# Kernel optimization log

Measured on AMD Instinct MI355X. Metric: run time of the kernel, lower is better.

## Reference

```python
import jax, jax.numpy as jnp
import numpy as np

LATENT_DIMENSION = 128
HIDDEN = 1024            # HIDDEN_SIZE + LATENT_DIMENSION
SONG_PIECE_SIZE = 128
SONG_LENGTH = 32768
T_STEPS = SONG_LENGTH // SONG_PIECE_SIZE  # 256
BATCH = 128


def setup_inputs() -> dict:
    key = jax.random.key(0)
    ks = jax.random.split(key, 7)
    s_ih = 1.0 / np.sqrt(HIDDEN)
    return {
        "current_batch_size": BATCH,
        "z": jax.random.normal(ks[0], (BATCH, 1, LATENT_DIMENSION), dtype=jnp.float32),
        "w_ih": jax.random.normal(ks[1], (4 * HIDDEN, LATENT_DIMENSION), dtype=jnp.float32) * s_ih,
        "w_hh": jax.random.normal(ks[2], (4 * HIDDEN, HIDDEN), dtype=jnp.float32) * s_ih,
        "b_ih": jax.random.normal(ks[3], (4 * HIDDEN,), dtype=jnp.float32) * s_ih,
        "b_hh": jax.random.normal(ks[4], (4 * HIDDEN,), dtype=jnp.float32) * s_ih,
        "W_fc": jax.random.normal(ks[5], (SONG_PIECE_SIZE, HIDDEN), dtype=jnp.float32) * s_ih,
        "b_fc": jax.random.normal(ks[6], (SONG_PIECE_SIZE,), dtype=jnp.float32) * s_ih,
    }


def _run(z, w_ih, w_hh, b_ih, b_hh, W_fc, b_fc):
    B = z.shape[0]
    # inputs per step: step 0 is z[:,0,:], remaining steps are zeros
    xs = jnp.concatenate(
        [z[:, 0:1, :].transpose(1, 0, 2),
         jnp.zeros((T_STEPS - 1, B, LATENT_DIMENSION), dtype=z.dtype)], axis=0)  # [T,B,L]
    h0 = jnp.zeros((B, HIDDEN), dtype=z.dtype)
    c0 = jnp.zeros((B, HIDDEN), dtype=z.dtype)

    def cell(carry, x):
        h, c = carry
        gates = x @ w_ih.T + b_ih + h @ w_hh.T + b_hh  # [B, 4H]
        i, f, g, o = jnp.split(gates, 4, axis=-1)       # PyTorch gate order i,f,g,o
        c_new = jax.nn.sigmoid(f) * c + jax.nn.sigmoid(i) * jnp.tanh(g)
        h_new = jax.nn.sigmoid(o) * jnp.tanh(c_new)
        y = h_new @ W_fc.T + b_fc                       # [B, SONG_PIECE_SIZE]
        return (h_new, c_new), y

    _, ys = jax.lax.scan(cell, (h0, c0), xs)            # ys: [T, B, P]
    return ys.transpose(1, 0, 2).reshape(B, SONG_LENGTH)


def reference(current_batch_size, z, w_ih, w_hh, b_ih, b_hh, W_fc, b_fc):
    return _run(z, w_ih, w_hh, b_ih, b_hh, W_fc, b_fc)
```

## Files before the change

kernel.cpp:

```cpp
#include <hip/hip_runtime.h>
#include <stdint.h>

#define BB   128
#define LL   128
#define HH   1024
#define G4   4096
#define TT   256
#define PP   128

#define NSL  64
#define NB   256
#define CARSL 56
#define FLS  32


typedef _Float16 half8  __attribute__((ext_vector_type(8)));
typedef float   floatx4 __attribute__((ext_vector_type(4)));

__device__ __forceinline__ float sigf(float x) {
  x = fminf(fmaxf(x, -30.f), 30.f);
  return 1.f / (1.f + __expf(-x));
}
__device__ __forceinline__ float tanhf_fast(float x) {
  x = fminf(fmaxf(x, -15.f), 15.f);
  float e = __expf(2.f * x);
  return (e - 1.f) / (e + 1.f);
}
__device__ __forceinline__ unsigned short f2h(float x) {
  _Float16 h = (_Float16)x;
  return __builtin_bit_cast(unsigned short, h);
}
__device__ __forceinline__ void store_h(unsigned short* p, float x) {
  __hip_atomic_store(p, f2h(x), __ATOMIC_RELAXED, __HIP_MEMORY_SCOPE_AGENT);
}

template <bool CACHED, int IMM>
__device__ __forceinline__ void ld16(half8& dst, const unsigned short* base) {
  if constexpr (CACHED)
    asm volatile("global_load_dwordx4 %0, %1, off offset:%2 sc0"
                 : "=&v"(dst) : "v"(base), "n"(IMM) : "memory");
  else
    asm volatile("global_load_dwordx4 %0, %1, off offset:%2 sc0 sc1"
                 : "=&v"(dst) : "v"(base), "n"(IMM) : "memory");
}

#define KSTEP(kc, WN)                                                      \
  {                                                                        \
    asm volatile("s_waitcnt vmcnt(%2)"                                     \
                 : "+v"(ap0[(kc) & 15]), "+v"(ap1[(kc) & 15]) : "n"(WN));  \
    half8 a0 = ap0[(kc) & 15], a1 = ap1[(kc) & 15];                        \
    const int sw = ((kc) * 4 + quad) ^ rsw;                                \
    _Pragma("unroll")                                                      \
    for (int nt = 0; nt < NT; ++nt) {                                      \
      half8 b = (nt < NGATE) ? w8[(nt * 16 + l15) * 128 + sw] : fcb[kc];   \
      acc[0][nt] = __builtin_amdgcn_mfma_f32_16x16x32_f16(a0, b, acc[0][nt], 0, 0, 0); \
      acc[1][nt] = __builtin_amdgcn_mfma_f32_16x16x32_f16(a1, b, acc[1][nt], 0, 0, 0); \
    }                                                                      \
    if ((kc) < 16) {                                                       \
      ld16<CACHED, ((kc) + 16) * 64>(ap0[(kc) & 15], p0);                  \
      ld16<CACHED, ((kc) + 16) * 64>(ap1[(kc) & 15], p1);                  \
    }                                                                      \
  }

__device__ __forceinline__ void publish(unsigned* qf, int sl, unsigned v, int lane) {
  asm volatile("s_waitcnt vmcnt(0)" ::: "memory");
  if (lane == 0)
    __hip_atomic_store(qf + sl * FLS, v, __ATOMIC_RELAXED, __HIP_MEMORY_SCOPE_AGENT);
}
__device__ __forceinline__ void waitq(const unsigned* qf, unsigned tgt, int lane) {
  const unsigned* p = qf + lane * FLS;
  int rounds = 0;
  for (;;) {
    unsigned v = __hip_atomic_load(p, __ATOMIC_RELAXED, __HIP_MEMORY_SCOPE_AGENT);
    if (__all(v >= tgt)) break;
    if (rounds < 2) __builtin_amdgcn_s_sleep(1);
    else            __builtin_amdgcn_s_sleep(8);
    ++rounds;
  }
}

__global__ void prep_gates0(const float* __restrict__ z, const float* __restrict__ w_ih,
                            const float* __restrict__ b_ih, const float* __restrict__ b_hh,
                            float* __restrict__ g0) {
  int j = blockIdx.x;
  int b = threadIdx.x;
  const float* zr = z + b * LL;
  const float* wr = w_ih + (size_t)j * LL;
  float s = 0.f;
#pragma unroll 4
  for (int k = 0; k < LL; ++k) s += zr[k] * wr[k];
  g0[(size_t)b * G4 + j] = s + b_ih[j] + b_hh[j];
}

__global__ void prep_weights(const float* __restrict__ w_hh,
                             unsigned short* __restrict__ wbuf) {
  int R = blockIdx.x;
  int sl = R >> 6, rr = R & 63, tile = rr >> 4, nl = rr & 15;
  int g = (tile == 0) ? 0 : (tile == 1) ? 2 : (tile == 2) ? 1 : 3;
  const float* src = w_hh + (size_t)(g * HH + sl * 16 + nl) * HH;
  int rsw = nl & 7;
  unsigned short* dst = wbuf + (size_t)R * HH;
  for (int k = threadIdx.x; k < HH; k += blockDim.x) {
    int dk = (((k >> 3) ^ rsw) << 3) | (k & 7);
    _Float16 v = (_Float16)src[k];
    dst[dk] = __builtin_bit_cast(unsigned short, v);
  }
}

template <bool CACHED, int NT, int NGATE>
__device__ __forceinline__ void gemmK(const unsigned short* __restrict__ hb,
                                      const half8* __restrict__ w8,
                                      const half8 (&fcb)[32],
                                      int au0, int au1,
                                      int quad, int rsw, int l15,
                                      floatx4 acc[2][NT]) {
  const unsigned short* p0 = hb + au0;
  const unsigned short* p1 = hb + au1;
  half8 ap0[16], ap1[16];
  ld16<CACHED, 0>(ap0[0], p0);     ld16<CACHED, 0>(ap1[0], p1);
  ld16<CACHED, 64>(ap0[1], p0);    ld16<CACHED, 64>(ap1[1], p1);
  ld16<CACHED, 128>(ap0[2], p0);   ld16<CACHED, 128>(ap1[2], p1);
  ld16<CACHED, 192>(ap0[3], p0);   ld16<CACHED, 192>(ap1[3], p1);
  ld16<CACHED, 256>(ap0[4], p0);   ld16<CACHED, 256>(ap1[4], p1);
  ld16<CACHED, 320>(ap0[5], p0);   ld16<CACHED, 320>(ap1[5], p1);
  ld16<CACHED, 384>(ap0[6], p0);   ld16<CACHED, 384>(ap1[6], p1);
  ld16<CACHED, 448>(ap0[7], p0);   ld16<CACHED, 448>(ap1[7], p1);
  ld16<CACHED, 512>(ap0[8], p0);   ld16<CACHED, 512>(ap1[8], p1);
  ld16<CACHED, 576>(ap0[9], p0);   ld16<CACHED, 576>(ap1[9], p1);
  ld16<CACHED, 640>(ap0[10], p0);  ld16<CACHED, 640>(ap1[10], p1);
  ld16<CACHED, 704>(ap0[11], p0);  ld16<CACHED, 704>(ap1[11], p1);
  ld16<CACHED, 768>(ap0[12], p0);  ld16<CACHED, 768>(ap1[12], p1);
  ld16<CACHED, 832>(ap0[13], p0);  ld16<CACHED, 832>(ap1[13], p1);
  ld16<CACHED, 896>(ap0[14], p0);  ld16<CACHED, 896>(ap1[14], p1);
  ld16<CACHED, 960>(ap0[15], p0);  ld16<CACHED, 960>(ap1[15], p1);
  KSTEP(0, 30)  KSTEP(1, 30)  KSTEP(2, 30)  KSTEP(3, 30)
  KSTEP(4, 30)  KSTEP(5, 30)  KSTEP(6, 30)  KSTEP(7, 30)
  KSTEP(8, 30)  KSTEP(9, 30)  KSTEP(10, 30) KSTEP(11, 30)
  KSTEP(12, 30) KSTEP(13, 30) KSTEP(14, 30) KSTEP(15, 30)
  KSTEP(16, 30) KSTEP(17, 28) KSTEP(18, 26) KSTEP(19, 24)
  KSTEP(20, 22) KSTEP(21, 20) KSTEP(22, 18) KSTEP(23, 16)
  KSTEP(24, 14) KSTEP(25, 12) KSTEP(26, 10) KSTEP(27, 8)
  KSTEP(28, 6)  KSTEP(29, 4)  KSTEP(30, 2)  KSTEP(31, 0)
}

template <bool CACHED>
__global__ __launch_bounds__(64, 1) void lstm_persist(
    const float* __restrict__ g0,
    const unsigned short* __restrict__ wbuf,
    const float* __restrict__ b_ih, const float* __restrict__ b_hh,
    const float* __restrict__ W_fc, const float* __restrict__ b_fc,
    float* __restrict__ out,
    unsigned short* __restrict__ hbuf,
    unsigned* __restrict__ ctl) {
  extern __shared__ __align__(16) unsigned short sW[];
  const int tid  = threadIdx.x;
  const int lane = tid;
  const int quad = lane >> 4;
  const int l15  = lane & 15;
  const int bid  = blockIdx.x;
  const int sl   = bid >> 2;
  const int q    = bid & 3;
  const int mbase = q * 32;
  const int rsw  = l15 & 7;
  const bool carrier = (sl >= CARSL);
  const int pcol = (sl - CARSL) * 16 + l15;

  unsigned* qf = ctl + q * (64 * FLS);

  {
    const uint4* s4 = (const uint4*)(wbuf + (size_t)sl * 64 * HH);
    uint4* d4 = (uint4*)sW;
    for (int i = tid; i < 64 * HH / 8; i += 64) d4[i] = s4[i];
  }
  __syncthreads();
  const half8* w8 = (const half8*)sW;
  const floatx4 z4 = {0.f, 0.f, 0.f, 0.f};

  half8 fcb[32];
  float biasf = 0.f;
  if (carrier) {
    biasf = b_fc[pcol];
    const float* wp = W_fc + (size_t)pcol * HH + quad * 8;
#pragma unroll
    for (int kc = 0; kc < 32; ++kc) {
      float4 f0 = *(const float4*)(wp + kc * 32);
      float4 f1 = *(const float4*)(wp + kc * 32 + 4);
      half8 hv;
      hv[0] = (_Float16)f0.x; hv[1] = (_Float16)f0.y;
      hv[2] = (_Float16)f0.z; hv[3] = (_Float16)f0.w;
      hv[4] = (_Float16)f1.x; hv[5] = (_Float16)f1.y;
      hv[6] = (_Float16)f1.z; hv[7] = (_Float16)f1.w;
      fcb[kc] = hv;
    }
  }

  const int u = sl * 16 + l15;
  const float bi = b_ih[u]          + b_hh[u];
  const float bf = b_ih[HH + u]     + b_hh[HH + u];
  const float bg = b_ih[2*HH + u]   + b_hh[2*HH + u];
  const float bo = b_ih[3*HH + u]   + b_hh[3*HH + u];
  float c[2][4] = {{0,0,0,0},{0,0,0,0}};

#pragma unroll
  for (int mt = 0; mt < 2; ++mt)
#pragma unroll
    for (int r = 0; r < 4; ++r) {
      const int m = mbase + mt * 16 + quad * 4 + r;
      const float* gr = g0 + (size_t)m * G4;
      float iv = gr[u], gv = gr[2 * HH + u], ov = gr[3 * HH + u];
      float ct = sigf(iv) * tanhf_fast(gv);
      c[mt][r] = ct;
      store_h(hbuf + (size_t)m * HH + u, sigf(ov) * tanhf_fast(ct));
    }
  publish(qf, sl, 1u, lane);

  const int au0 = (mbase +      l15) * HH + quad * 8;
  const int au1 = (mbase + 16 + l15) * HH + quad * 8;

  if (carrier) {
    for (int t = 1; t < TT; ++t) {
      waitq(qf, (unsigned)t, lane);
      const unsigned short* hb = hbuf +
          (size_t)(CACHED ? (t - 1) : ((t - 1) & 1)) * BB * HH;
      unsigned short* hw = hbuf + (size_t)(CACHED ? t : (t & 1)) * BB * HH;
      floatx4 acc[2][5] = {{z4, z4, z4, z4, z4}, {z4, z4, z4, z4, z4}};
      gemmK<CACHED, 5, 4>(hb, w8, fcb, au0, au1, quad, rsw, l15, acc);
      float yv[2][4];
#pragma unroll
      for (int mt = 0; mt < 2; ++mt)
#pragma unroll
        for (int r = 0; r < 4; ++r) {
          float iv = sigf(acc[mt][0][r] + bi);
          float gv = tanhf_fast(acc[mt][1][r] + bg);
          float fv = sigf(acc[mt][2][r] + bf);
          float ov = sigf(acc[mt][3][r] + bo);
          float ct = fv * c[mt][r] + iv * gv;
          c[mt][r] = ct;
          const int m = mbase + mt * 16 + quad * 4 + r;
          store_h(hw + (size_t)m * HH + u, ov * tanhf_fast(ct));
          yv[mt][r] = acc[mt][4][r] + biasf;
        }
      publish(qf, sl, (unsigned)(t + 1), lane);
#pragma unroll
      for (int mt = 0; mt < 2; ++mt)
#pragma unroll
        for (int r = 0; r < 4; ++r) {
          const int m = mbase + mt * 16 + quad * 4 + r;
          out[(size_t)m * (TT * PP) + (size_t)(t - 1) * PP + pcol] = yv[mt][r];
        }
    }
    waitq(qf, (unsigned)TT, lane);
    {
      const unsigned short* hb = hbuf +
          (size_t)(CACHED ? (TT - 1) : ((TT - 1) & 1)) * BB * HH;
      floatx4 acc[2][1] = {{z4}, {z4}};
      gemmK<CACHED, 1, 0>(hb, w8, fcb, au0, au1, quad, rsw, l15, acc);
#pragma unroll
      for (int mt = 0; mt < 2; ++mt)
#pragma unroll
        for (int r = 0; r < 4; ++r) {
          const int m = mbase + mt * 16 + quad * 4 + r;
          out[(size_t)m * (TT * PP) + (size_t)(TT - 1) * PP + pcol] =
              acc[mt][0][r] + biasf;
        }
    }
  } else {
    for (int t = 1; t < TT; ++t) {
      waitq(qf, (unsigned)t, lane);
      const unsigned short* hb = hbuf +
          (size_t)(CACHED ? (t - 1) : ((t - 1) & 1)) * BB * HH;
      unsigned short* hw = hbuf + (size_t)(CACHED ? t : (t & 1)) * BB * HH;
      floatx4 acc[2][4] = {{z4, z4, z4, z4}, {z4, z4, z4, z4}};
      gemmK<CACHED, 4, 4>(hb, w8, fcb, au0, au1, quad, rsw, l15, acc);
#pragma unroll
      for (int mt = 0; mt < 2; ++mt)
#pragma unroll
        for (int r = 0; r < 4; ++r) {
          float iv = sigf(acc[mt][0][r] + bi);
          float gv = tanhf_fast(acc[mt][1][r] + bg);
          float fv = sigf(acc[mt][2][r] + bf);
          float ov = sigf(acc[mt][3][r] + bo);
          float ct = fv * c[mt][r] + iv * gv;
          c[mt][r] = ct;
          const int m = mbase + mt * 16 + quad * 4 + r;
          store_h(hw + (size_t)m * HH + u, ov * tanhf_fast(ct));
        }
      publish(qf, sl, (unsigned)(t + 1), lane);
    }
  }
}

extern "C" void kernel_launch(void* const* d_in, const int* in_sizes, int n_in,
                              void* d_out, int out_size, void* d_ws, size_t ws_size,
                              hipStream_t stream) {
  const float* z    = (const float*)d_in[1];
  const float* w_ih = (const float*)d_in[2];
  const float* w_hh = (const float*)d_in[3];
  const float* b_ih = (const float*)d_in[4];
  const float* b_hh = (const float*)d_in[5];
  const float* W_fc = (const float*)d_in[6];
  const float* b_fc = (const float*)d_in[7];
  float* out = (float*)d_out;

  const size_t ctlB   = 65536;
  const size_t hFull  = (size_t)TT * BB * HH * 2;
  const size_t hMin   = (size_t)2  * BB * HH * 2;
  const size_t g0B    = (size_t)BB * G4 * 4;
  const size_t wbufB  = (size_t)NSL * 64 * HH * 2;
  const bool cached = ws_size >= ctlB + hFull + g0B + wbufB;
  const size_t hB = cached ? hFull : hMin;

  char* ws = (char*)d_ws;
  unsigned*       ctl  = (unsigned*)ws;
  unsigned short* hbuf = (unsigned short*)(ws + ctlB);
  float*          g0   = (float*)(ws + ctlB + hB);
  unsigned short* wbuf = (unsigned short*)(ws + ctlB + hB + g0B);

  (void)hipFuncSetAttribute(reinterpret_cast<const void*>(lstm_persist<true>),
                            hipFuncAttributeMaxDynamicSharedMemorySize, 160 * 1024);
  (void)hipFuncSetAttribute(reinterpret_cast<const void*>(lstm_persist<false>),
                            hipFuncAttributeMaxDynamicSharedMemorySize, 160 * 1024);

  hipMemsetAsync(ctl, 0, ctlB, stream);
  prep_gates0 <<<dim3(G4), dim3(BB), 0, stream>>>(z, w_ih, b_ih, b_hh, g0);
  prep_weights<<<dim3(NSL * 64), dim3(256), 0, stream>>>(w_hh, wbuf);
  if (cached)
    lstm_persist<true><<<dim3(NB), dim3(64), 128 * 1024, stream>>>(
        g0, wbuf, b_ih, b_hh, W_fc, b_fc, out, hbuf, ctl);
  else
    lstm_persist<false><<<dim3(NB), dim3(64), 128 * 1024, stream>>>(
        g0, wbuf, b_ih, b_hh, W_fc, b_fc, out, hbuf, ctl);
}
```

Baseline: 2.182 ms.

## Split per-step barrier into K-quarter waits with rotated start offsets

```diff
diff --git a/kernel.cpp b/kernel.cpp
--- a/kernel.cpp
+++ b/kernel.cpp
@@ -12,6 +12,7 @@
 #define NB   256
 #define CARSL 56
 #define FLS  32
+#define HROW 2048
 
 
 typedef _Float16 half8  __attribute__((ext_vector_type(8)));
@@ -34,41 +35,23 @@
   __hip_atomic_store(p, f2h(x), __ATOMIC_RELAXED, __HIP_MEMORY_SCOPE_AGENT);
 }
 
-template <bool CACHED, int IMM>
+template <int IMM>
 __device__ __forceinline__ void ld16(half8& dst, const unsigned short* base) {
-  if constexpr (CACHED)
-    asm volatile("global_load_dwordx4 %0, %1, off offset:%2 sc0"
-                 : "=&v"(dst) : "v"(base), "n"(IMM) : "memory");
-  else
-    asm volatile("global_load_dwordx4 %0, %1, off offset:%2 sc0 sc1"
-                 : "=&v"(dst) : "v"(base), "n"(IMM) : "memory");
-}
-
-#define KSTEP(kc, WN)                                                      \
-  {                                                                        \
-    asm volatile("s_waitcnt vmcnt(%2)"                                     \
-                 : "+v"(ap0[(kc) & 15]), "+v"(ap1[(kc) & 15]) : "n"(WN));  \
-    half8 a0 = ap0[(kc) & 15], a1 = ap1[(kc) & 15];                        \
-    const int sw = ((kc) * 4 + quad) ^ rsw;                                \
-    _Pragma("unroll")                                                      \
-    for (int nt = 0; nt < NT; ++nt) {                                      \
-      half8 b = (nt < NGATE) ? w8[(nt * 16 + l15) * 128 + sw] : fcb[kc];   \
-      acc[0][nt] = __builtin_amdgcn_mfma_f32_16x16x32_f16(a0, b, acc[0][nt], 0, 0, 0); \
-      acc[1][nt] = __builtin_amdgcn_mfma_f32_16x16x32_f16(a1, b, acc[1][nt], 0, 0, 0); \
-    }                                                                      \
-    if ((kc) < 16) {                                                       \
-      ld16<CACHED, ((kc) + 16) * 64>(ap0[(kc) & 15], p0);                  \
-      ld16<CACHED, ((kc) + 16) * 64>(ap1[(kc) & 15], p1);                  \
-    }                                                                      \
-  }
+  asm volatile("global_load_dwordx4 %0, %1, off offset:%2 sc0 sc1"
+               : "=&v"(dst) : "v"(base), "n"(IMM) : "memory");
+}
+#define FLD(dst, ptr)                                                      \
+  asm volatile("global_load_dword %0, %1, off sc0 sc1"                     \
+               : "=&v"(dst) : "v"(ptr) : "memory")
 
 __device__ __forceinline__ void publish(unsigned* qf, int sl, unsigned v, int lane) {
   asm volatile("s_waitcnt vmcnt(0)" ::: "memory");
   if (lane == 0)
     __hip_atomic_store(qf + sl * FLS, v, __ATOMIC_RELAXED, __HIP_MEMORY_SCOPE_AGENT);
 }
-__device__ __forceinline__ void waitq(const unsigned* qf, unsigned tgt, int lane) {
-  const unsigned* p = qf + lane * FLS;
+__device__ __forceinline__ void wait01(const unsigned* qf, int g0q, unsigned tgt, int lane) {
+  const int idx = ((g0q + (lane >> 5)) & 3) * 16 + (lane & 15);
+  const unsigned* p = qf + idx * FLS;
   int rounds = 0;
   for (;;) {
     unsigned v = __hip_atomic_load(p, __ATOMIC_RELAXED, __HIP_MEMORY_SCOPE_AGENT);
@@ -76,6 +59,24 @@
     if (rounds < 2) __builtin_amdgcn_s_sleep(1);
     else            __builtin_amdgcn_s_sleep(8);
     ++rounds;
+  }
+}
+__device__ __forceinline__ void waitg(const unsigned* qf, int g0q, int s,
+                                      unsigned tgt, int lane) {
+  const int idx = ((g0q + s) & 3) * 16 + (lane & 15);
+  const unsigned* p = qf + idx * FLS;
+  for (;;) {
+    unsigned v = __hip_atomic_load(p, __ATOMIC_RELAXED, __HIP_MEMORY_SCOPE_AGENT);
+    if (__all(v >= tgt)) break;
+    __builtin_amdgcn_s_sleep(1);
+  }
+}
+__device__ __forceinline__ void waitq(const unsigned* qf, unsigned tgt, int lane) {
+  const unsigned* p = qf + lane * FLS;
+  for (;;) {
+    unsigned v = __hip_atomic_load(p, __ATOMIC_RELAXED, __HIP_MEMORY_SCOPE_AGENT);
+    if (__all(v >= tgt)) break;
+    __builtin_amdgcn_s_sleep(1);
   }
 }
 
@@ -107,43 +108,79 @@
   }
 }
 
-template <bool CACHED, int NT, int NGATE>
-__device__ __forceinline__ void gemmK(const unsigned short* __restrict__ hb,
+#define KBODY(j)                                                           \
+  {                                                                        \
+    half8 a0 = ap0[(j) & 15], a1 = ap1[(j) & 15];                          \
+    const int sw = (((r0 + (j) * 4) & 127) + quad) ^ rsw;                  \
+    _Pragma("unroll")                                                      \
+    for (int nt = 0; nt < NT; ++nt) {                                      \
+      half8 b = (nt < NGATE) ? w8[(nt * 16 + l15) * 128 + sw] : fcb[j];    \
+      acc[0][nt] = __builtin_amdgcn_mfma_f32_16x16x32_f16(a0, b, acc[0][nt], 0, 0, 0); \
+      acc[1][nt] = __builtin_amdgcn_mfma_f32_16x16x32_f16(a1, b, acc[1][nt], 0, 0, 0); \
+    }                                                                      \
+    if ((j) < 16) {                                                        \
+      ld16<((j) + 16) * 64>(ap0[(j) & 15], p0);                            \
+      ld16<((j) + 16) * 64>(ap1[(j) & 15], p1);                            \
+    }                                                                      \
+  }
+#define KSTEPR(j, WN)                                                      \
+  {                                                                        \
+    asm volatile("s_waitcnt vmcnt(%2)"                                     \
+                 : "+v"(ap0[(j) & 15]), "+v"(ap1[(j) & 15]) : "n"(WN));    \
+    KBODY(j)                                                               \
+  }
+
+template <int NT, int NGATE>
+__device__ __forceinline__ void gemmP(const unsigned short* __restrict__ hb,
                                       const half8* __restrict__ w8,
                                       const half8 (&fcb)[32],
-                                      int au0, int au1,
-                                      int quad, int rsw, int l15,
+                                      int au0, int au1, int quad, int rsw,
+                                      int l15, int r0, int g0q,
+                                      const unsigned* qf, unsigned tgt, int lane,
                                       floatx4 acc[2][NT]) {
   const unsigned short* p0 = hb + au0;
   const unsigned short* p1 = hb + au1;
+  unsigned fv2, fv3;
+  {
+    const unsigned* f2p = qf + (((g0q + 2) & 3) * 16 + (lane & 15)) * FLS;
+    const unsigned* f3p = qf + (((g0q + 3) & 3) * 16 + (lane & 15)) * FLS;
+    FLD(fv2, f2p);
+    FLD(fv3, f3p);
+  }
   half8 ap0[16], ap1[16];
-  ld16<CACHED, 0>(ap0[0], p0);     ld16<CACHED, 0>(ap1[0], p1);
-  ld16<CACHED, 64>(ap0[1], p0);    ld16<CACHED, 64>(ap1[1], p1);
-  ld16<CACHED, 128>(ap0[2], p0);   ld16<CACHED, 128>(ap1[2], p1);
-  ld16<CACHED, 192>(ap0[3], p0);   ld16<CACHED, 192>(ap1[3], p1);
-  ld16<CACHED, 256>(ap0[4], p0);   ld16<CACHED, 256>(ap1[4], p1);
-  ld16<CACHED, 320>(ap0[5], p0);   ld16<CACHED, 320>(ap1[5], p1);
-  ld16<CACHED, 384>(ap0[6], p0);   ld16<CACHED, 384>(ap1[6], p1);
-  ld16<CACHED, 448>(ap0[7], p0);   ld16<CACHED, 448>(ap1[7], p1);
-  ld16<CACHED, 512>(ap0[8], p0);   ld16<CACHED, 512>(ap1[8], p1);
-  ld16<CACHED, 576>(ap0[9], p0);   ld16<CACHED, 576>(ap1[9], p1);
-  ld16<CACHED, 640>(ap0[10], p0);  ld16<CACHED, 640>(ap1[10], p1);
-  ld16<CACHED, 704>(ap0[11], p0);  ld16<CACHED, 704>(ap1[11], p1);
-  ld16<CACHED, 768>(ap0[12], p0);  ld16<CACHED, 768>(ap1[12], p1);
-  ld16<CACHED, 832>(ap0[13], p0);  ld16<CACHED, 832>(ap1[13], p1);
-  ld16<CACHED, 896>(ap0[14], p0);  ld16<CACHED, 896>(ap1[14], p1);
-  ld16<CACHED, 960>(ap0[15], p0);  ld16<CACHED, 960>(ap1[15], p1);
-  KSTEP(0, 30)  KSTEP(1, 30)  KSTEP(2, 30)  KSTEP(3, 30)
-  KSTEP(4, 30)  KSTEP(5, 30)  KSTEP(6, 30)  KSTEP(7, 30)
-  KSTEP(8, 30)  KSTEP(9, 30)  KSTEP(10, 30) KSTEP(11, 30)
-  KSTEP(12, 30) KSTEP(13, 30) KSTEP(14, 30) KSTEP(15, 30)
-  KSTEP(16, 30) KSTEP(17, 28) KSTEP(18, 26) KSTEP(19, 24)
-  KSTEP(20, 22) KSTEP(21, 20) KSTEP(22, 18) KSTEP(23, 16)
-  KSTEP(24, 14) KSTEP(25, 12) KSTEP(26, 10) KSTEP(27, 8)
-  KSTEP(28, 6)  KSTEP(29, 4)  KSTEP(30, 2)  KSTEP(31, 0)
-}
-
-template <bool CACHED>
+  ld16<0>(ap0[0], p0);     ld16<0>(ap1[0], p1);
+  ld16<64>(ap0[1], p0);    ld16<64>(ap1[1], p1);
+  ld16<128>(ap0[2], p0);   ld16<128>(ap1[2], p1);
+  ld16<192>(ap0[3], p0);   ld16<192>(ap1[3], p1);
+  ld16<256>(ap0[4], p0);   ld16<256>(ap1[4], p1);
+  ld16<320>(ap0[5], p0);   ld16<320>(ap1[5], p1);
+  ld16<384>(ap0[6], p0);   ld16<384>(ap1[6], p1);
+  ld16<448>(ap0[7], p0);   ld16<448>(ap1[7], p1);
+  ld16<512>(ap0[8], p0);   ld16<512>(ap1[8], p1);
+  ld16<576>(ap0[9], p0);   ld16<576>(ap1[9], p1);
+  ld16<640>(ap0[10], p0);  ld16<640>(ap1[10], p1);
+  ld16<704>(ap0[11], p0);  ld16<704>(ap1[11], p1);
+  ld16<768>(ap0[12], p0);  ld16<768>(ap1[12], p1);
+  ld16<832>(ap0[13], p0);  ld16<832>(ap1[13], p1);
+  ld16<896>(ap0[14], p0);  ld16<896>(ap1[14], p1);
+  ld16<960>(ap0[15], p0);  ld16<960>(ap1[15], p1);
+  asm volatile("s_waitcnt vmcnt(30)"
+               : "+v"(ap0[0]), "+v"(ap1[0]), "+v"(fv2), "+v"(fv3));
+  if (!__all(fv2 >= tgt)) waitg(qf, g0q, 2, tgt, lane);
+  KBODY(0)
+  KSTEPR(1, 30)  KSTEPR(2, 30)  KSTEPR(3, 30)
+  KSTEPR(4, 30)  KSTEPR(5, 30)  KSTEPR(6, 30)  KSTEPR(7, 30)
+  asm volatile("s_waitcnt vmcnt(30)" : "+v"(ap0[8]), "+v"(ap1[8]));
+  if (!__all(fv3 >= tgt)) waitg(qf, g0q, 3, tgt, lane);
+  KBODY(8)
+  KSTEPR(9, 30)  KSTEPR(10, 30) KSTEPR(11, 30)
+  KSTEPR(12, 30) KSTEPR(13, 30) KSTEPR(14, 30) KSTEPR(15, 30)
+  KSTEPR(16, 30) KSTEPR(17, 28) KSTEPR(18, 26) KSTEPR(19, 24)
+  KSTEPR(20, 22) KSTEPR(21, 20) KSTEPR(22, 18) KSTEPR(23, 16)
+  KSTEPR(24, 14) KSTEPR(25, 12) KSTEPR(26, 10) KSTEPR(27, 8)
+  KSTEPR(28, 6)  KSTEPR(29, 4)  KSTEPR(30, 2)  KSTEPR(31, 0)
+}
+
 __global__ __launch_bounds__(64, 1) void lstm_persist(
     const float* __restrict__ g0,
     const unsigned short* __restrict__ wbuf,
@@ -162,6 +199,8 @@
   const int q    = bid & 3;
   const int mbase = q * 32;
   const int rsw  = l15 & 7;
+  const int g0q  = sl >> 4;
+  const int r0   = g0q * 32;
   const bool carrier = (sl >= CARSL);
   const int pcol = (sl - CARSL) * 16 + l15;
 
@@ -182,15 +221,16 @@
     biasf = b_fc[pcol];
     const float* wp = W_fc + (size_t)pcol * HH + quad * 8;
 #pragma unroll
-    for (int kc = 0; kc < 32; ++kc) {
-      float4 f0 = *(const float4*)(wp + kc * 32);
-      float4 f1 = *(const float4*)(wp + kc * 32 + 4);
+    for (int j = 0; j < 32; ++j) {
+      const int phys = (g0q * 8 + j) & 31;
+      float4 f0 = *(const float4*)(wp + phys * 32);
+      float4 f1 = *(const float4*)(wp + phys * 32 + 4);
       half8 hv;
       hv[0] = (_Float16)f0.x; hv[1] = (_Float16)f0.y;
       hv[2] = (_Float16)f0.z; hv[3] = (_Float16)f0.w;
       hv[4] = (_Float16)f1.x; hv[5] = (_Float16)f1.y;
       hv[6] = (_Float16)f1.z; hv[7] = (_Float16)f1.w;
-      fcb[kc] = hv;
+      fcb[j] = hv;
     }
   }
 
@@ -210,21 +250,23 @@
       float iv = gr[u], gv = gr[2 * HH + u], ov = gr[3 * HH + u];
       float ct = sigf(iv) * tanhf_fast(gv);
       c[mt][r] = ct;
-      store_h(hbuf + (size_t)m * HH + u, sigf(ov) * tanhf_fast(ct));
+      float hv = sigf(ov) * tanhf_fast(ct);
+      store_h(hbuf + (size_t)m * HROW + u, hv);
+      store_h(hbuf + (size_t)m * HROW + 1024 + u, hv);
     }
   publish(qf, sl, 1u, lane);
 
-  const int au0 = (mbase +      l15) * HH + quad * 8;
-  const int au1 = (mbase + 16 + l15) * HH + quad * 8;
+  const int au0 = (mbase +      l15) * HROW + g0q * 256 + quad * 8;
+  const int au1 = (mbase + 16 + l15) * HROW + g0q * 256 + quad * 8;
 
   if (carrier) {
     for (int t = 1; t < TT; ++t) {
-      waitq(qf, (unsigned)t, lane);
-      const unsigned short* hb = hbuf +
-          (size_t)(CACHED ? (t - 1) : ((t - 1) & 1)) * BB * HH;
-      unsigned short* hw = hbuf + (size_t)(CACHED ? t : (t & 1)) * BB * HH;
+      wait01(qf, g0q, (unsigned)t, lane);
+      const unsigned short* hb = hbuf + (size_t)((t - 1) & 1) * BB * HROW;
+      unsigned short* hw = hbuf + (size_t)(t & 1) * BB * HROW;
       floatx4 acc[2][5] = {{z4, z4, z4, z4, z4}, {z4, z4, z4, z4, z4}};
-      gemmK<CACHED, 5, 4>(hb, w8, fcb, au0, au1, quad, rsw, l15, acc);
+      gemmP<5, 4>(hb, w8, fcb, au0, au1, quad, rsw, l15, r0, g0q, qf,
+                  (unsigned)t, lane, acc);
       float yv[2][4];
 #pragma unroll
       for (int mt = 0; mt < 2; ++mt)
@@ -237,7 +279,9 @@
           float ct = fv * c[mt][r] + iv * gv;
           c[mt][r] = ct;
           const int m = mbase + mt * 16 + quad * 4 + r;
-          store_h(hw + (size_t)m * HH + u, ov * tanhf_fast(ct));
+          float hv = ov * tanhf_fast(ct);
+          store_h(hw + (size_t)m * HROW + u, hv);
+          store_h(hw + (size_t)m * HROW + 1024 + u, hv);
           yv[mt][r] = acc[mt][4][r] + biasf;
         }
       publish(qf, sl, (unsigned)(t + 1), lane);
@@ -251,10 +295,10 @@
     }
     waitq(qf, (unsigned)TT, lane);
     {
-      const unsigned short* hb = hbuf +
-          (size_t)(CACHED ? (TT - 1) : ((TT - 1) & 1)) * BB * HH;
+      const unsigned short* hb = hbuf + (size_t)((TT - 1) & 1) * BB * HROW;
       floatx4 acc[2][1] = {{z4}, {z4}};
-      gemmK<CACHED, 1, 0>(hb, w8, fcb, au0, au1, quad, rsw, l15, acc);
+      gemmP<1, 0>(hb, w8, fcb, au0, au1, quad, rsw, l15, r0, g0q, qf,
+                  (unsigned)TT, lane, acc);
 #pragma unroll
       for (int mt = 0; mt < 2; ++mt)
 #pragma unroll
@@ -266,12 +310,12 @@
     }
   } else {
     for (int t = 1; t < TT; ++t) {
-      waitq(qf, (unsigned)t, lane);
-      const unsigned short* hb = hbuf +
-          (size_t)(CACHED ? (t - 1) : ((t - 1) & 1)) * BB * HH;
-      unsigned short* hw = hbuf + (size_t)(CACHED ? t : (t & 1)) * BB * HH;
+      wait01(qf, g0q, (unsigned)t, lane);
+      const unsigned short* hb = hbuf + (size_t)((t - 1) & 1) * BB * HROW;
+      unsigned short* hw = hbuf + (size_t)(t & 1) * BB * HROW;
       floatx4 acc[2][4] = {{z4, z4, z4, z4}, {z4, z4, z4, z4}};
-      gemmK<CACHED, 4, 4>(hb, w8, fcb, au0, au1, quad, rsw, l15, acc);
+      gemmP<4, 4>(hb, w8, fcb, au0, au1, quad, rsw, l15, r0, g0q, qf,
+                  (unsigned)t, lane, acc);
 #pragma unroll
       for (int mt = 0; mt < 2; ++mt)
 #pragma unroll
@@ -283,7 +327,9 @@
           float ct = fv * c[mt][r] + iv * gv;
           c[mt][r] = ct;
           const int m = mbase + mt * 16 + quad * 4 + r;
-          store_h(hw + (size_t)m * HH + u, ov * tanhf_fast(ct));
+          float hv = ov * tanhf_fast(ct);
+          store_h(hw + (size_t)m * HROW + u, hv);
+          store_h(hw + (size_t)m * HROW + 1024 + u, hv);
         }
       publish(qf, sl, (unsigned)(t + 1), lane);
     }
@@ -302,32 +348,21 @@
   const float* b_fc = (const float*)d_in[7];
   float* out = (float*)d_out;
 
-  const size_t ctlB   = 65536;
-  const size_t hFull  = (size_t)TT * BB * HH * 2;
-  const size_t hMin   = (size_t)2  * BB * HH * 2;
-  const size_t g0B    = (size_t)BB * G4 * 4;
-  const size_t wbufB  = (size_t)NSL * 64 * HH * 2;
-  const bool cached = ws_size >= ctlB + hFull + g0B + wbufB;
-  const size_t hB = cached ? hFull : hMin;
-
+  const size_t ctlB  = 65536;
+  const size_t hB    = (size_t)2 * BB * HROW * 2;
+  const size_t g0B   = (size_t)BB * G4 * 4;
   char* ws = (char*)d_ws;
   unsigned*       ctl  = (unsigned*)ws;
   unsigned short* hbuf = (unsigned short*)(ws + ctlB);
   float*          g0   = (float*)(ws + ctlB + hB);
   unsigned short* wbuf = (unsigned short*)(ws + ctlB + hB + g0B);
 
-  (void)hipFuncSetAttribute(reinterpret_cast<const void*>(lstm_persist<true>),
-                            hipFuncAttributeMaxDynamicSharedMemorySize, 160 * 1024);
-  (void)hipFuncSetAttribute(reinterpret_cast<const void*>(lstm_persist<false>),
+  (void)hipFuncSetAttribute(reinterpret_cast<const void*>(lstm_persist),
                             hipFuncAttributeMaxDynamicSharedMemorySize, 160 * 1024);
 
   hipMemsetAsync(ctl, 0, ctlB, stream);
   prep_gates0 <<<dim3(G4), dim3(BB), 0, stream>>>(z, w_ih, b_ih, b_hh, g0);
   prep_weights<<<dim3(NSL * 64), dim3(256), 0, stream>>>(w_hh, wbuf);
-  if (cached)
-    lstm_persist<true><<<dim3(NB), dim3(64), 128 * 1024, stream>>>(
-        g0, wbuf, b_ih, b_hh, W_fc, b_fc, out, hbuf, ctl);
-  else
-    lstm_persist<false><<<dim3(NB), dim3(64), 128 * 1024, stream>>>(
-        g0, wbuf, b_ih, b_hh, W_fc, b_fc, out, hbuf, ctl);
-}
+  lstm_persist<<<dim3(NB), dim3(64), 128 * 1024, stream>>>(g0, wbuf, b_ih, b_hh,
+                                                           W_fc, b_fc, out, hbuf, ctl);
+}
```

After: 2.162 ms. About the same (-0.9%).
